# Kernel tuning notes

Hardware: AMD Instinct MI355X
Metric: run time of the kernel (lower is better)

## Reference

```python
import jax, jax.numpy as jnp
import numpy as np

B, T, E, H, V = 128, 32, 512, 1024, 32000


def setup_inputs() -> dict:
    key = jax.random.key(0)
    ks = jax.random.split(key, 9)
    s = 0.02
    return {
        "features": jax.random.normal(ks[0], (B, H), dtype=jnp.float32),
        "captions": jax.random.randint(ks[1], (B, T), 0, V, dtype=jnp.int64),
        "embed_table": jax.random.normal(ks[2], (V, E), dtype=jnp.float32) * s,
        "W_ih": jax.random.normal(ks[3], (4 * H, E), dtype=jnp.float32) * s,
        "W_hh": jax.random.normal(ks[4], (4 * H, H), dtype=jnp.float32) * s,
        "b_ih": jax.random.normal(ks[5], (4 * H,), dtype=jnp.float32) * s,
        "b_hh": jax.random.normal(ks[6], (4 * H,), dtype=jnp.float32) * s,
        "fc_W": jax.random.normal(ks[7], (V, H), dtype=jnp.float32) * s,
        "fc_b": jax.random.normal(ks[8], (V,), dtype=jnp.float32) * s,
    }


def reference(features, captions, embed_table, W_ih, W_hh, b_ih, b_hh, fc_W, fc_b):
    # init_hidden: h0 = c0 = features (single layer)
    h0 = features  # [B, H]
    c0 = features
    # embed all captions, then step over first T-1 tokens
    x_seq = embed_table[captions[:, : T - 1]]  # [B, T-1, E]
    x_seq = jnp.transpose(x_seq, (1, 0, 2))    # [T-1, B, E]

    def step(carry, x_t):
        h, c = carry
        gates = x_t @ W_ih.T + h @ W_hh.T + b_ih + b_hh  # [B, 4H]
        i, f, g, o = jnp.split(gates, 4, axis=-1)         # torch gate order i,f,g,o
        i = jax.nn.sigmoid(i)
        f = jax.nn.sigmoid(f)
        g = jnp.tanh(g)
        o = jax.nn.sigmoid(o)
        c_new = f * c + i * g
        h_new = o * jnp.tanh(c_new)
        logits = h_new @ fc_W.T + fc_b  # [B, V]
        return (h_new, c_new), logits

    _, outs = jax.lax.scan(step, (h0, c0), x_seq)  # outs: [T-1, B, V]
    outs = jnp.transpose(outs, (1, 0, 2))          # [B, T-1, V]
    # outputs[:, 0, :] stays zero; outputs[:, t+1, :] = step t
    zero0 = jnp.zeros((features.shape[0], 1, fc_W.shape[0]), dtype=outs.dtype)
    return jnp.concatenate([zero0, outs], axis=1)  # [B, T, V]
```

## Files before the change

### kernel.cpp

```cpp
#include <hip/hip_runtime.h>
#include <hip/hip_bf16.h>
#include <cstdint>


typedef unsigned short u16;
typedef __attribute__((ext_vector_type(8))) short bf16x8;
typedef __attribute__((ext_vector_type(4))) float f32x4;

static constexpr int B_ = 128, T_ = 32, E_ = 512, H_ = 1024, V_ = 32000;
static constexpr int TS = T_ - 1;
static constexpr int M_SEQ = TS * B_;
static constexpr int G4 = 4 * H_;

__device__ __forceinline__ u16 f2bf(float x) {
  union { __hip_bfloat16 b; u16 u; } c; c.b = __float2bfloat16(x); return c.u;
}

__device__ __forceinline__ void gload_lds16(const void* g, void* l) {
  __builtin_amdgcn_global_load_lds(
      (const __attribute__((address_space(1))) unsigned int*)g,
      (__attribute__((address_space(3))) unsigned int*)l, 16, 0, 0);
}

__device__ __forceinline__ float sigm(float x) { return 1.f / (1.f + expf(-x)); }


__global__ void cvt_bf16x4(const float* __restrict__ s, u16* __restrict__ d, int n) {
  int i = (blockIdx.x * blockDim.x + threadIdx.x) * 4;
  if (i >= n) return;
  const float4 v = *(const float4*)(s + i);
  *(ushort4*)(d + i) = make_ushort4(f2bf(v.x), f2bf(v.y), f2bf(v.z), f2bf(v.w));
}

__global__ void addb(const float* __restrict__ a, const float* __restrict__ b,
                     float* __restrict__ o) {
  int i = blockIdx.x * blockDim.x + threadIdx.x;
  if (i < G4) o[i] = a[i] + b[i];
}

__global__ void gather_x(const int* __restrict__ cap, const float* __restrict__ emb,
                         u16* __restrict__ X) {
  int i4 = blockIdx.x * blockDim.x + threadIdx.x;
  if (i4 >= M_SEQ * (E_ / 4)) return;
  int i = i4 * 4;
  int tb = i >> 9;
  int e = i & (E_ - 1);
  int t = tb >> 7;
  int b = tb & 127;
  int row = cap[b * T_ + t];
  const float4 v = *(const float4*)(emb + (long)row * E_ + e);
  *(ushort4*)(X + i) = make_ushort4(f2bf(v.x), f2bf(v.y), f2bf(v.z), f2bf(v.w));
}

__global__ void hc_init(const float* __restrict__ f, u16* __restrict__ h,
                        float* __restrict__ c) {
  int i = blockIdx.x * blockDim.x + threadIdx.x;
  if (i < B_ * H_) { float v = f[i]; h[i] = f2bf(v); c[i] = v; }
}

__global__ void zero_t0(float* __restrict__ out) {
  int i4 = blockIdx.x * blockDim.x + threadIdx.x;
  if (i4 >= B_ * (V_ / 4)) return;
  int b = i4 / (V_ / 4), v4 = i4 % (V_ / 4);
  *(float4*)(out + (long)b * T_ * V_ + v4 * 4) = make_float4(0.f, 0.f, 0.f, 0.f);
}


template<int SCATTER>
__global__ __launch_bounds__(256)
void gemm_bt(const u16* __restrict__ A, int lda,
             const u16* __restrict__ B, int ldb,
             float* __restrict__ C, long ldc,
             const float* __restrict__ bias,
             int K, int ntn)
{
  constexpr int BM = 128, BN = 128, NFR = 4;
  const int bid = blockIdx.x;
  const int mt = bid / ntn, nt = bid % ntn;
  const int tid = threadIdx.x;
  const int wid = tid >> 6, lane = tid & 63;
  const int wm = (wid >> 1) * 64, wn = (wid & 1) * 64;
  const int l15 = lane & 15, l4 = lane >> 4;

  __shared__ __align__(16) u16 As[BM * 32];
  __shared__ __align__(16) u16 Bs[BN * 32];

  f32x4 acc[4][NFR] = {};

  const u16* Ag = A + (long)(mt * BM + (tid >> 2)) * lda + (tid & 3) * 8;
  const u16* Bg = B + (long)(nt * BN + (tid >> 2)) * ldb + (tid & 3) * 8;
  char* AsW = (char*)As + wid * 1024;
  char* BsW = (char*)Bs + wid * 1024;

  for (int kt = 0; kt < K; kt += 32) {
    gload_lds16(Ag + kt, AsW);
    gload_lds16(Ag + 64 * (long)lda + kt, AsW + 4096);
    gload_lds16(Bg + kt, BsW);
    gload_lds16(Bg + 64 * (long)ldb + kt, BsW + 4096);
    __syncthreads();

    const u16* Ab = As + (wm + l15) * 32 + l4 * 8;
    const u16* Bb = Bs + (wn + l15) * 32 + l4 * 8;
    bf16x8 af[4], bfr[NFR];
#pragma unroll
    for (int i = 0; i < 4; ++i) af[i] = *(const bf16x8*)(Ab + i * 16 * 32);
#pragma unroll
    for (int j = 0; j < NFR; ++j) bfr[j] = *(const bf16x8*)(Bb + j * 16 * 32);
#pragma unroll
    for (int i = 0; i < 4; ++i)
#pragma unroll
      for (int j = 0; j < NFR; ++j)
        acc[i][j] = __builtin_amdgcn_mfma_f32_16x16x32_bf16(af[i], bfr[j], acc[i][j], 0, 0, 0);
    __syncthreads();
  }

  const int grow0 = mt * BM + wm + l4 * 4;
  const int gcol0 = nt * BN + wn + l15;
#pragma unroll
  for (int i = 0; i < 4; ++i) {
#pragma unroll
    for (int j = 0; j < NFR; ++j) {
      const int col = gcol0 + j * 16;
      const float bv = bias ? bias[col] : 0.0f;
#pragma unroll
      for (int r = 0; r < 4; ++r) {
        const int row = grow0 + i * 16 + r;
        float v = acc[i][j][r] + bv;
        long o;
        if constexpr (SCATTER) {
          const int t = row >> 7, b = row & 127;
          o = ((long)(b * T_ + t + 1)) * ldc + col;
        } else {
          o = (long)row * ldc + col;
        }
        C[o] = v;
      }
    }
  }
}


__global__ __launch_bounds__(256)
void lstm_step(const u16* __restrict__ h_in,
               const u16* __restrict__ Whh,
               const float* __restrict__ gx,
               float* __restrict__ c,
               u16* __restrict__ h_out,
               u16* __restrict__ hseq)
{
  const int tid = threadIdx.x;
  const int wid = tid >> 6, lane = tid & 63;
  const int l15 = lane & 15, l4 = lane >> 4;
  const int j0 = blockIdx.x * 16;

  __shared__ __align__(16) u16 As[128 * 32];
  __shared__ __align__(16) u16 Bs[64 * 32];

  f32x4 acc[2][4] = {};

  const u16* Ag = h_in + (long)(tid >> 2) * H_ + (tid & 3) * 8;
  const int vr = tid >> 2;
  const u16* Bg = Whh + (long)((vr >> 4) * H_ + j0 + (vr & 15)) * H_ + (tid & 3) * 8;
  char* AsW = (char*)As + wid * 1024;
  char* BsW = (char*)Bs + wid * 1024;

  for (int kt = 0; kt < H_; kt += 32) {
    gload_lds16(Ag + kt, AsW);
    gload_lds16(Ag + 64 * H_ + kt, AsW + 4096);
    gload_lds16(Bg + kt, BsW);
    __syncthreads();

    const u16* Ab = As + (wid * 32 + l15) * 32 + l4 * 8;
    const u16* Bb = Bs + l15 * 32 + l4 * 8;
    bf16x8 af[2], bfr[4];
#pragma unroll
    for (int i = 0; i < 2; ++i) af[i] = *(const bf16x8*)(Ab + i * 16 * 32);
#pragma unroll
    for (int g = 0; g < 4; ++g) bfr[g] = *(const bf16x8*)(Bb + g * 16 * 32);
#pragma unroll
    for (int i = 0; i < 2; ++i)
#pragma unroll
      for (int g = 0; g < 4; ++g)
        acc[i][g] = __builtin_amdgcn_mfma_f32_16x16x32_bf16(af[i], bfr[g], acc[i][g], 0, 0, 0);
    __syncthreads();
  }

  const int j = j0 + l15;
#pragma unroll
  for (int mi = 0; mi < 2; ++mi) {
#pragma unroll
    for (int r = 0; r < 4; ++r) {
      const int m = wid * 32 + mi * 16 + l4 * 4 + r;
      const float* gr = gx + (long)m * G4 + j;
      float gi = sigm(acc[mi][0][r] + gr[0]);
      float gf = sigm(acc[mi][1][r] + gr[H_]);
      float gg = tanhf(acc[mi][2][r] + gr[2 * H_]);
      float go = sigm(acc[mi][3][r] + gr[3 * H_]);
      const int idx = m * H_ + j;
      float cn = gf * c[idx] + gi * gg;
      c[idx] = cn;
      u16 hb = f2bf(go * tanhf(cn));
      h_out[idx] = hb;
      hseq[idx] = hb;
    }
  }
}


extern "C" void kernel_launch(void* const* d_in, const int* in_sizes, int n_in,
                              void* d_out, int out_size, void* d_ws, size_t ws_size,
                              hipStream_t stream) {
  const float* features = (const float*)d_in[0];
  const int*   captions = (const int*)d_in[1];
  const float* embed    = (const float*)d_in[2];
  const float* W_ih     = (const float*)d_in[3];
  const float* W_hh     = (const float*)d_in[4];
  const float* b_ih     = (const float*)d_in[5];
  const float* b_hh     = (const float*)d_in[6];
  const float* fc_W     = (const float*)d_in[7];
  const float* fc_b     = (const float*)d_in[8];
  float* out = (float*)d_out;

  size_t off = 0;
  auto alloc = [&](size_t bytes) {
    void* p = (char*)d_ws + off;
    off += (bytes + 255) & ~(size_t)255;
    return p;
  };
  u16*  Wih_b = (u16*)alloc((size_t)G4 * E_ * 2);
  u16*  Whh_b = (u16*)alloc((size_t)G4 * H_ * 2);
  u16*  fcW_b = (u16*)alloc((size_t)V_ * H_ * 2);
  u16*  Xb    = (u16*)alloc((size_t)M_SEQ * E_ * 2);
  u16*  Hseq  = (u16*)alloc((size_t)M_SEQ * H_ * 2);
  u16*  hb0   = (u16*)alloc((size_t)B_ * H_ * 2);
  u16*  hb1   = (u16*)alloc((size_t)B_ * H_ * 2);
  float* cst  = (float*)alloc((size_t)B_ * H_ * 4);
  float* Gx   = (float*)alloc((size_t)M_SEQ * G4 * 4);
  float* bsum = (float*)alloc((size_t)G4 * 4);
  if (off > ws_size) return;

  cvt_bf16x4<<<(G4 * E_ / 4 + 255) / 256, 256, 0, stream>>>(W_ih, Wih_b, G4 * E_);
  cvt_bf16x4<<<(G4 * H_ / 4 + 255) / 256, 256, 0, stream>>>(W_hh, Whh_b, G4 * H_);
  cvt_bf16x4<<<(V_ * H_ / 4 + 255) / 256, 256, 0, stream>>>(fc_W, fcW_b, V_ * H_);
  addb<<<(G4 + 255) / 256, 256, 0, stream>>>(b_ih, b_hh, bsum);
  gather_x<<<(M_SEQ * E_ / 4 + 255) / 256, 256, 0, stream>>>(captions, embed, Xb);
  hc_init<<<(B_ * H_ + 255) / 256, 256, 0, stream>>>(features, hb0, cst);
  zero_t0<<<(B_ * V_ / 4 + 255) / 256, 256, 0, stream>>>(out);

  gemm_bt<0><<<(M_SEQ / 128) * (G4 / 128), 256, 0, stream>>>(
      Xb, E_, Wih_b, E_, Gx, G4, bsum, E_, G4 / 128);

  u16* hp[2] = { hb0, hb1 };
  for (int t = 0; t < TS; ++t) {
    lstm_step<<<H_ / 16, 256, 0, stream>>>(
        hp[t & 1], Whh_b, Gx + (size_t)t * B_ * G4, cst, hp[(t + 1) & 1],
        Hseq + (size_t)t * B_ * H_);
  }

  gemm_bt<1><<<(M_SEQ / 128) * (V_ / 128), 256, 0, stream>>>(
      Hseq, H_, fcW_b, H_, out, V_, fc_b, H_, V_ / 128);
}
```

Baseline: 1.682 ms.

## Fuse LSTM timesteps into one persistent kernel with grid barrier

Replaces the 31 per-timestep lstm_step launches with a single persistent kernel of 64 blocks that loops over timesteps, synchronising through an atomic-counter grid barrier and keeping cell state in registers. The inner K loop gains a 4-deep LDS ring with swizzled addressing and explicit waitcnt pipelining. The output GEMM gets an XCD-aware grouped tile order for better L2 reuse. It removes launch overhead and global c traffic, but relies on all 64 blocks being co-resident for the spin barrier.

Measured after the change: 1.746 ms. 1.04x slower.

```diff
diff --git a/kernel.cpp b/kernel.cpp
--- a/kernel.cpp
+++ b/kernel.cpp
@@ -11,6 +11,7 @@
 static constexpr int TS = T_ - 1;
 static constexpr int M_SEQ = TS * B_;
 static constexpr int G4 = 4 * H_;
+static constexpr int NBLK = 64;
 
 __device__ __forceinline__ u16 f2bf(float x) {
   union { __hip_bfloat16 b; u16 u; } c; c.b = __float2bfloat16(x); return c.u;
@@ -53,9 +54,10 @@
 }
 
 __global__ void hc_init(const float* __restrict__ f, u16* __restrict__ h,
-                        float* __restrict__ c) {
+                        unsigned* __restrict__ ctr) {
   int i = blockIdx.x * blockDim.x + threadIdx.x;
-  if (i < B_ * H_) { float v = f[i]; h[i] = f2bf(v); c[i] = v; }
+  if (i == 0) *ctr = 0u;
+  if (i < B_ * H_) h[i] = f2bf(f[i]);
 }
 
 __global__ void zero_t0(float* __restrict__ out) {
@@ -66,7 +68,7 @@
 }
 
 
-template<int SCATTER>
+template<int SCATTER, int ORDER>
 __global__ __launch_bounds__(256)
 void gemm_bt(const u16* __restrict__ A, int lda,
              const u16* __restrict__ B, int ldb,
@@ -75,8 +77,23 @@
              int K, int ntn)
 {
   constexpr int BM = 128, BN = 128, NFR = 4;
-  const int bid = blockIdx.x;
-  const int mt = bid / ntn, nt = bid % ntn;
+  int mt, nt;
+  if constexpr (ORDER == 1) {
+    const int nwg = gridDim.x;
+    const int nmt = nwg / ntn;
+    const int xcd = blockIdx.x & 7, o = blockIdx.x >> 3;
+    const int q = nwg >> 3, rr = nwg & 7;
+    const int swz = (xcd < rr ? xcd * (q + 1) : rr * (q + 1) + (xcd - rr) * q) + o;
+    constexpr int GM = 8;
+    const int npg = GM * ntn;
+    const int grp = swz / npg;
+    const int first = grp * GM;
+    const int gsz = min(GM, nmt - first);
+    mt = first + (swz % npg) % gsz;
+    nt = (swz % npg) / gsz;
+  } else {
+    mt = blockIdx.x / ntn; nt = blockIdx.x % ntn;
+  }
   const int tid = threadIdx.x;
   const int wid = tid >> 6, lane = tid & 63;
   const int wm = (wid >> 1) * 64, wn = (wid & 1) * 64;
@@ -140,69 +157,106 @@
 }
 
 
+__device__ __forceinline__ void gridbar(unsigned* ctr, unsigned target, int tid) {
+  __builtin_amdgcn_fence(__ATOMIC_RELEASE, "agent");
+  __syncthreads();
+  if (tid == 0) {
+    __hip_atomic_fetch_add(ctr, 1u, __ATOMIC_RELAXED, __HIP_MEMORY_SCOPE_AGENT);
+    while (__hip_atomic_load(ctr, __ATOMIC_RELAXED, __HIP_MEMORY_SCOPE_AGENT) < target)
+      __builtin_amdgcn_s_sleep(2);
+  }
+  __syncthreads();
+  __builtin_amdgcn_fence(__ATOMIC_ACQUIRE, "agent");
+}
+
 __global__ __launch_bounds__(256)
-void lstm_step(const u16* __restrict__ h_in,
-               const u16* __restrict__ Whh,
-               const float* __restrict__ gx,
-               float* __restrict__ c,
-               u16* __restrict__ h_out,
-               u16* __restrict__ hseq)
+void lstm_persist(const u16* __restrict__ h0,
+                  const u16* __restrict__ Whh,
+                  const float* __restrict__ feat,
+                  const float* __restrict__ gx,
+                  u16* __restrict__ Hseq,
+                  unsigned* __restrict__ ctr)
 {
   const int tid = threadIdx.x;
   const int wid = tid >> 6, lane = tid & 63;
   const int l15 = lane & 15, l4 = lane >> 4;
   const int j0 = blockIdx.x * 16;
-
-  __shared__ __align__(16) u16 As[128 * 32];
-  __shared__ __align__(16) u16 Bs[64 * 32];
-
-  f32x4 acc[2][4] = {};
-
-  const u16* Ag = h_in + (long)(tid >> 2) * H_ + (tid & 3) * 8;
-  const int vr = tid >> 2;
-  const u16* Bg = Whh + (long)((vr >> 4) * H_ + j0 + (vr & 15)) * H_ + (tid & 3) * 8;
-  char* AsW = (char*)As + wid * 1024;
-  char* BsW = (char*)Bs + wid * 1024;
-
-  for (int kt = 0; kt < H_; kt += 32) {
-    gload_lds16(Ag + kt, AsW);
-    gload_lds16(Ag + 64 * H_ + kt, AsW + 4096);
-    gload_lds16(Bg + kt, BsW);
-    __syncthreads();
-
-    const u16* Ab = As + (wid * 32 + l15) * 32 + l4 * 8;
-    const u16* Bb = Bs + l15 * 32 + l4 * 8;
-    bf16x8 af[2], bfr[4];
-#pragma unroll
-    for (int i = 0; i < 2; ++i) af[i] = *(const bf16x8*)(Ab + i * 16 * 32);
-#pragma unroll
-    for (int g = 0; g < 4; ++g) bfr[g] = *(const bf16x8*)(Bb + g * 16 * 32);
-#pragma unroll
-    for (int i = 0; i < 2; ++i)
+  const int jj = j0 + l15;
+
+  __shared__ __align__(16) u16 As[4][128 * 32];
+  __shared__ __align__(16) u16 Bs[4][64 * 32];
+
+  float creg[2][4];
+#pragma unroll
+  for (int mi = 0; mi < 2; ++mi)
+#pragma unroll
+    for (int r = 0; r < 4; ++r)
+      creg[mi][r] = feat[(wid * 32 + mi * 16 + l4 * 4 + r) * H_ + jj];
+
+  const int src_kk = (((lane & 3) ^ ((lane >> 3) & 3))) * 8;
+  const long a_off = (long)(32 * wid + (lane >> 2)) * H_ + src_kk;
+  const int br = tid >> 2;
+  const long b_off = (long)((br >> 4) * H_ + j0 + (br & 15)) * H_ + src_kk;
+  const int rd_sx = (l4 ^ ((l15 >> 1) & 3)) * 16;
+
+  for (int t = 0; t < TS; ++t) {
+    const u16* hsrc = (t == 0) ? h0 : Hseq + (size_t)(t - 1) * B_ * H_;
+    const float* gxt = gx + (size_t)t * B_ * G4;
+
+    f32x4 acc[2][4] = {};
+
+    auto stage = [&](int kt2) {
+      char* Ad = (char*)As[kt2 & 3] + wid * 2048;
+      gload_lds16(hsrc + a_off + kt2 * 32, Ad);
+      gload_lds16(hsrc + a_off + 16 * H_ + kt2 * 32, Ad + 1024);
+      gload_lds16(Whh + b_off + kt2 * 32, (char*)Bs[kt2 & 3] + wid * 1024);
+    };
+
+    stage(0);
+    stage(1);
+
+#pragma unroll
+    for (int kt = 0; kt < 32; ++kt) {
+      if (kt + 2 < 32) stage(kt + 2);
+      if (kt < 30)       asm volatile("s_waitcnt vmcnt(6) lgkmcnt(0)" ::: "memory");
+      else if (kt == 30) asm volatile("s_waitcnt vmcnt(3) lgkmcnt(0)" ::: "memory");
+      else               asm volatile("s_waitcnt vmcnt(0) lgkmcnt(0)" ::: "memory");
+      asm volatile("s_barrier" ::: "memory");
+
+      const char* Ab = (const char*)As[kt & 3];
+      const char* Bb = (const char*)Bs[kt & 3];
+      bf16x8 af[2], bfr[4];
+#pragma unroll
+      for (int mi = 0; mi < 2; ++mi)
+        af[mi] = *(const bf16x8*)(Ab + (32 * wid + mi * 16 + l15) * 64 + rd_sx);
 #pragma unroll
       for (int g = 0; g < 4; ++g)
-        acc[i][g] = __builtin_amdgcn_mfma_f32_16x16x32_bf16(af[i], bfr[g], acc[i][g], 0, 0, 0);
-    __syncthreads();
-  }
-
-  const int j = j0 + l15;
-#pragma unroll
-  for (int mi = 0; mi < 2; ++mi) {
-#pragma unroll
-    for (int r = 0; r < 4; ++r) {
-      const int m = wid * 32 + mi * 16 + l4 * 4 + r;
-      const float* gr = gx + (long)m * G4 + j;
-      float gi = sigm(acc[mi][0][r] + gr[0]);
-      float gf = sigm(acc[mi][1][r] + gr[H_]);
-      float gg = tanhf(acc[mi][2][r] + gr[2 * H_]);
-      float go = sigm(acc[mi][3][r] + gr[3 * H_]);
-      const int idx = m * H_ + j;
-      float cn = gf * c[idx] + gi * gg;
-      c[idx] = cn;
-      u16 hb = f2bf(go * tanhf(cn));
-      h_out[idx] = hb;
-      hseq[idx] = hb;
+        bfr[g] = *(const bf16x8*)(Bb + (g * 16 + l15) * 64 + rd_sx);
+#pragma unroll
+      for (int mi = 0; mi < 2; ++mi)
+#pragma unroll
+        for (int g = 0; g < 4; ++g)
+          acc[mi][g] = __builtin_amdgcn_mfma_f32_16x16x32_bf16(af[mi], bfr[g], acc[mi][g], 0, 0, 0);
     }
+
+    u16* hrow = Hseq + (size_t)t * B_ * H_;
+#pragma unroll
+    for (int mi = 0; mi < 2; ++mi) {
+#pragma unroll
+      for (int r = 0; r < 4; ++r) {
+        const int m = wid * 32 + mi * 16 + l4 * 4 + r;
+        const float* gr = gxt + (long)m * G4 + jj;
+        float gi = sigm(acc[mi][0][r] + gr[0]);
+        float gf = sigm(acc[mi][1][r] + gr[H_]);
+        float gg = tanhf(acc[mi][2][r] + gr[2 * H_]);
+        float go = sigm(acc[mi][3][r] + gr[3 * H_]);
+        float cn = gf * creg[mi][r] + gi * gg;
+        creg[mi][r] = cn;
+        hrow[m * H_ + jj] = f2bf(go * tanhf(cn));
+      }
+    }
+
+    if (t != TS - 1) gridbar(ctr, (unsigned)((t + 1) * NBLK), tid);
   }
 }
 
@@ -233,10 +287,9 @@
   u16*  Xb    = (u16*)alloc((size_t)M_SEQ * E_ * 2);
   u16*  Hseq  = (u16*)alloc((size_t)M_SEQ * H_ * 2);
   u16*  hb0   = (u16*)alloc((size_t)B_ * H_ * 2);
-  u16*  hb1   = (u16*)alloc((size_t)B_ * H_ * 2);
-  float* cst  = (float*)alloc((size_t)B_ * H_ * 4);
   float* Gx   = (float*)alloc((size_t)M_SEQ * G4 * 4);
   float* bsum = (float*)alloc((size_t)G4 * 4);
+  unsigned* ctr = (unsigned*)alloc(256);
   if (off > ws_size) return;
 
   cvt_bf16x4<<<(G4 * E_ / 4 + 255) / 256, 256, 0, stream>>>(W_ih, Wih_b, G4 * E_);
@@ -244,19 +297,14 @@
   cvt_bf16x4<<<(V_ * H_ / 4 + 255) / 256, 256, 0, stream>>>(fc_W, fcW_b, V_ * H_);
   addb<<<(G4 + 255) / 256, 256, 0, stream>>>(b_ih, b_hh, bsum);
   gather_x<<<(M_SEQ * E_ / 4 + 255) / 256, 256, 0, stream>>>(captions, embed, Xb);
-  hc_init<<<(B_ * H_ + 255) / 256, 256, 0, stream>>>(features, hb0, cst);
+  hc_init<<<(B_ * H_ + 255) / 256, 256, 0, stream>>>(features, hb0, ctr);
   zero_t0<<<(B_ * V_ / 4 + 255) / 256, 256, 0, stream>>>(out);
 
-  gemm_bt<0><<<(M_SEQ / 128) * (G4 / 128), 256, 0, stream>>>(
+  gemm_bt<0, 0><<<(M_SEQ / 128) * (G4 / 128), 256, 0, stream>>>(
       Xb, E_, Wih_b, E_, Gx, G4, bsum, E_, G4 / 128);
 
-  u16* hp[2] = { hb0, hb1 };
-  for (int t = 0; t < TS; ++t) {
-    lstm_step<<<H_ / 16, 256, 0, stream>>>(
-        hp[t & 1], Whh_b, Gx + (size_t)t * B_ * G4, cst, hp[(t + 1) & 1],
-        Hseq + (size_t)t * B_ * H_);
-  }
-
-  gemm_bt<1><<<(M_SEQ / 128) * (V_ / 128), 256, 0, stream>>>(
+  lstm_persist<<<NBLK, 256, 0, stream>>>(hb0, Whh_b, features, Gx, Hseq, ctr);
+
+  gemm_bt<1, 1><<<(M_SEQ / 128) * (V_ / 128), 256, 0, stream>>>(
       Hseq, H_, fcW_b, H_, out, V_, fc_b, H_, V_ / 128);
 }
```
